# Optimization experiments

Measured on AMD Instinct MI355X. Metric: run time of the kernel, lower is better.

The kernel has to match this reference:

```python
import math
import jax, jax.numpy as jnp
import numpy as np

B, L, H, E = 16, 2048, 8, 64
FACTOR = 1


def setup_inputs() -> dict:
    key = jax.random.key(0)
    kq, kk, kv = jax.random.split(key, 3)
    queries = jax.random.normal(kq, (B, L, H, E), dtype=jnp.float32)
    keys = jax.random.normal(kk, (B, L, H, E), dtype=jnp.float32)
    values = jax.random.normal(kv, (B, L, H, E), dtype=jnp.float32)
    return {"queries": queries, "keys": keys, "values": values, "attn_mask": 0}


def reference(queries, keys, values, attn_mask):
    # queries/keys/values: [B, L, H, E]; attn_mask is unused (as in the original).
    b, l, h, e = queries.shape
    # [B, H, E, L]
    qp = jnp.transpose(queries, (0, 2, 3, 1))
    kp = jnp.transpose(keys, (0, 2, 3, 1))
    vp = jnp.transpose(values, (0, 2, 3, 1))

    # Period-based dependency discovery via FFT cross-correlation.
    qf = jnp.fft.rfft(qp, axis=-1)
    kf = jnp.fft.rfft(kp, axis=-1)
    corr = jnp.fft.irfft(qf * jnp.conj(kf), n=l, axis=-1)  # [B, H, E, L]

    # Inference-style time-delay aggregation (per-batch top-k delays).
    top_k = max(1, int(FACTOR * math.log(l)))
    mean_value = corr.mean(axis=(1, 2))  # [B, L]
    weights, delay = jax.lax.top_k(mean_value, top_k)  # [B, K]
    tmp_corr = jax.nn.softmax(weights, axis=-1)  # [B, K]

    # Gather from doubled tensor == circular roll: index (t + delay) mod L.
    idx = (jnp.arange(l)[None, None, :] + delay[:, :, None]) % l  # [B, K, L]
    # vp[:, None]: [B, 1, H, E, L]; idx broadcast to [B, K, 1, 1, L]
    pattern = jnp.take_along_axis(vp[:, None], idx[:, :, None, None, :], axis=-1)  # [B, K, H, E, L]
    agg = jnp.einsum('bkhel,bk->bhel', pattern, tmp_corr)  # [B, H, E, L]

    return jnp.transpose(agg, (0, 3, 1, 2))  # [B, L, H, E]
```

## Files before the change

kernel.cpp:

```cpp
#include <hip/hip_runtime.h>
#include <hip/hip_fp16.h>
#include <cstdint>
#include <cstddef>

#define BB 16
#define LL 2048
#define CC 512
#define TK 7
#define PDC(a) ((a) + ((a) >> 4))
#define PSTR 1056
#define NG 128

typedef float2 cf;
typedef __attribute__((ext_vector_type(4))) float f32x4v;

__device__ inline cf cadd(cf a, cf b){ return make_float2(a.x + b.x, a.y + b.y); }
__device__ inline cf csub(cf a, cf b){ return make_float2(a.x - b.x, a.y - b.y); }
__device__ inline cf cmul(cf a, cf b){ return make_float2(a.x*b.x - a.y*b.y, a.x*b.y + a.y*b.x); }

template<int S> __device__ inline cf crot(cf z){
  return (S < 0) ? make_float2(z.y, -z.x) : make_float2(-z.y, z.x);
}

template<int S> __device__ inline void dft4(cf* x){
  const cf t0 = cadd(x[0], x[2]), t1 = csub(x[0], x[2]);
  const cf t2 = cadd(x[1], x[3]), t3 = csub(x[1], x[3]);
  const cf r = crot<S>(t3);
  x[0] = cadd(t0, t2); x[2] = csub(t0, t2);
  x[1] = cadd(t1, r);  x[3] = csub(t1, r);
}

template<int S> __device__ inline void dft8(cf* x){
  cf e[4] = { x[0], x[2], x[4], x[6] };
  cf o[4] = { x[1], x[3], x[5], x[7] };
  dft4<S>(e); dft4<S>(o);
  const float H = 0.70710678118654752440f;
  o[1] = cmul(o[1], make_float2(H, (float)S * H));
  o[2] = crot<S>(o[2]);
  o[3] = cmul(o[3], make_float2(-H, (float)S * H));
  x[0] = cadd(e[0], o[0]); x[4] = csub(e[0], o[0]);
  x[1] = cadd(e[1], o[1]); x[5] = csub(e[1], o[1]);
  x[2] = cadd(e[2], o[2]); x[6] = csub(e[2], o[2]);
  x[3] = cadd(e[3], o[3]); x[7] = csub(e[3], o[3]);
}

struct Tw { cf w2[7], w3[7], w4a[3], w4b[3]; };

template<int S>
__device__ inline void make_tw(int tid, Tw& T){
  const float base = (float)S * 6.283185307179586f / 2048.0f;
  const int j7 = tid & 7, j63 = tid & 63;
#pragma unroll
  for (int i = 0; i < 7; ++i){
    float s, c;
    __sincosf(base * (float)(32 * (i + 1) * j7), &s, &c);  T.w2[i] = make_float2(c, s);
    __sincosf(base * (float)( 4 * (i + 1) * j63), &s, &c); T.w3[i] = make_float2(c, s);
  }
#pragma unroll
  for (int i = 0; i < 3; ++i){
    float s, c;
    __sincosf(base * (float)((i + 1) * tid), &s, &c);         T.w4a[i] = make_float2(c, s);
    __sincosf(base * (float)((i + 1) * (tid + 256)), &s, &c); T.w4b[i] = make_float2(c, s);
  }
}

template<int S>
__device__ inline void fft_s123(cf* Bc, cf* Cc, cf* x, const Tw& T, int tid){
  dft8<S>(x);
#pragma unroll
  for (int t = 0; t < 8; ++t) Bc[PDC((tid << 3) + t)] = x[t];
  __syncthreads();
  {
    cf y[8];
#pragma unroll
    for (int t = 0; t < 8; ++t) y[t] = Bc[PDC(tid + (t << 8))];
#pragma unroll
    for (int t = 1; t < 8; ++t) y[t] = cmul(y[t], T.w2[t - 1]);
    dft8<S>(y);
    const int base = ((tid >> 3) << 6) + (tid & 7);
#pragma unroll
    for (int t = 0; t < 8; ++t) Cc[PDC(base + (t << 3))] = y[t];
  }
  __syncthreads();
  {
    cf y[8];
#pragma unroll
    for (int t = 0; t < 8; ++t) y[t] = Cc[PDC(tid + (t << 8))];
#pragma unroll
    for (int t = 1; t < 8; ++t) y[t] = cmul(y[t], T.w3[t - 1]);
    dft8<S>(y);
    const int base = ((tid >> 6) << 9) + (tid & 63);
#pragma unroll
    for (int t = 0; t < 8; ++t) Bc[PDC(base + (t << 6))] = y[t];
  }
  __syncthreads();
}

__global__ __launch_bounds__(256) void transpose_pack(const float* __restrict__ q,
                                                      const float* __restrict__ k,
                                                      __half2* __restrict__ z){
  int bid = blockIdx.x;
  const int tt = bid & 31; bid >>= 5;
  const int ct = bid & 7;  bid >>= 3;
  const int b = bid;
  const int t0 = tt << 6, c0 = ct << 6;
  __shared__ __half2 T[64][69];
  const int tid = threadIdx.x;
  const size_t inbase = ((size_t)b * LL + t0) * CC + c0;
  const int c4 = (tid & 15) << 2;
  f32x4v a[4], e[4];
#pragma unroll
  for (int p2 = 0; p2 < 4; ++p2){
    const int row = (p2 << 4) + (tid >> 4);
    a[p2] = __builtin_nontemporal_load(
        reinterpret_cast<const f32x4v*>(q + inbase + (size_t)row * CC + c4));
    e[p2] = __builtin_nontemporal_load(
        reinterpret_cast<const f32x4v*>(k + inbase + (size_t)row * CC + c4));
  }
#pragma unroll
  for (int p2 = 0; p2 < 4; ++p2){
    const int row = (p2 << 4) + (tid >> 4);
    T[row][c4 + 0] = __floats2half2_rn(a[p2][0], e[p2][0]);
    T[row][c4 + 1] = __floats2half2_rn(a[p2][1], e[p2][1]);
    T[row][c4 + 2] = __floats2half2_rn(a[p2][2], e[p2][2]);
    T[row][c4 + 3] = __floats2half2_rn(a[p2][3], e[p2][3]);
  }
  __syncthreads();
  const size_t outbase = ((size_t)b * CC + c0) * LL + (size_t)t0;
#pragma unroll
  for (int it = 0; it < 4; ++it){
    const int idx = (it << 8) + tid;
    const int c = idx >> 4;
    const int t4 = (idx & 15) << 2;
    const __half2 u0 = T[t4 + 0][c], u1 = T[t4 + 1][c];
    const __half2 u2 = T[t4 + 2][c], u3 = T[t4 + 3][c];
    uint4 w;
    w.x = *reinterpret_cast<const uint*>(&u0);
    w.y = *reinterpret_cast<const uint*>(&u1);
    w.z = *reinterpret_cast<const uint*>(&u2);
    w.w = *reinterpret_cast<const uint*>(&u3);
    *reinterpret_cast<uint4*>(&z[outbase + (size_t)c * LL + t4]) = w;
  }
}

__global__ __launch_bounds__(256) void fft_fwd(const __half2* __restrict__ z,
                                               float2* __restrict__ Ppart){
  int bid = blockIdx.x;
  const int g = bid & (NG - 1); const int b = bid >> 7;
  const int tid = threadIdx.x;
  __shared__ cf B[2176];
  Tw T; make_tw<-1>(tid, T);
  const __half2* zg = z + (((size_t)b * CC + (size_t)g * 4) << 11);
  float accRe[4] = {0,0,0,0};
  float accIm[4] = {0,0,0,0};
  float acc1024 = 0.f;
  __half2 h[8];
#pragma unroll
  for (int t = 0; t < 8; ++t) h[t] = zg[tid + (t << 8)];
  for (int ch = 0; ch < 4; ++ch){
    cf x[8];
#pragma unroll
    for (int t = 0; t < 8; ++t) x[t] = __half22float2(h[t]);
    if (ch < 3){
      const __half2* zn = zg + ((size_t)(ch + 1) << 11);
#pragma unroll
      for (int t = 0; t < 8; ++t) h[t] = zn[tid + (t << 8)];
    }
    dft8<-1>(x);
    __syncthreads();
#pragma unroll
    for (int t = 0; t < 8; ++t) B[PDC((tid << 3) + t)] = x[t];
    __syncthreads();
    cf y[8];
#pragma unroll
    for (int t = 0; t < 8; ++t) y[t] = B[PDC(tid + (t << 8))];
#pragma unroll
    for (int t = 1; t < 8; ++t) y[t] = cmul(y[t], T.w2[t - 1]);
    dft8<-1>(y);
    __syncthreads();
    {
      const int base = ((tid >> 3) << 6) + (tid & 7);
#pragma unroll
      for (int t = 0; t < 8; ++t) B[PDC(base + (t << 3))] = y[t];
    }
    __syncthreads();
#pragma unroll
    for (int t = 0; t < 8; ++t) y[t] = B[PDC(tid + (t << 8))];
#pragma unroll
    for (int t = 1; t < 8; ++t) y[t] = cmul(y[t], T.w3[t - 1]);
    dft8<-1>(y);
    __syncthreads();
    {
      const int base = ((tid >> 6) << 9) + (tid & 63);
#pragma unroll
      for (int t = 0; t < 8; ++t) B[PDC(base + (t << 6))] = y[t];
    }
    __syncthreads();
    cf y0[4], y1[4];
#pragma unroll
    for (int t = 0; t < 4; ++t) y0[t] = B[PDC(tid + (t << 9))];
#pragma unroll
    for (int t = 0; t < 4; ++t) y1[t] = B[PDC(tid + 256 + (t << 9))];
#pragma unroll
    for (int t = 1; t < 4; ++t){
      y0[t] = cmul(y0[t], T.w4a[t - 1]);
      y1[t] = cmul(y1[t], T.w4b[t - 1]);
    }
    dft4<-1>(y0); dft4<-1>(y1);
#pragma unroll
    for (int t = 0; t < 4; ++t) B[PDC(tid + (t << 9))] = y0[t];
#pragma unroll
    for (int t = 0; t < 4; ++t) B[PDC(tid + 256 + (t << 9))] = y1[t];
    __syncthreads();
    const cf Areg[4] = { y0[0], y1[0], y0[1], y1[1] };
#pragma unroll
    for (int r = 0; r < 4; ++r){
      const int f = tid + (r << 8);
      const int p = (2048 - f) & 2047;
      const cf A = Areg[r];
      const cf Bv = B[PDC(p)];
      accRe[r] += 0.5f  * (Bv.y * A.x + Bv.x * A.y);
      accIm[r] += 0.25f * (A.x * A.x + A.y * A.y - Bv.x * Bv.x - Bv.y * Bv.y);
    }
    if (tid == 0){
      const cf A = y0[2];
      acc1024 += A.x * A.y;
    }
  }
  float2* pp = Ppart + ((size_t)b * NG + g) * PSTR;
#pragma unroll
  for (int r = 0; r < 4; ++r)
    pp[tid + (r << 8)] = make_float2(accRe[r], accIm[r]);
  if (tid == 0) pp[1024] = make_float2(acc1024, 0.f);
}

__global__ __launch_bounds__(256) void reduce_P(const float2* __restrict__ Ppart,
                                                float2* __restrict__ P){
  const int gid = blockIdx.x * 256 + threadIdx.x;
  const int b = gid >> 11, f = gid & 2047;
  const int src = (f <= 1024) ? f : 2048 - f;
  const float sgn = (f <= 1024) ? 1.f : -1.f;
  float sr = 0.f, si = 0.f;
#pragma unroll 8
  for (int g = 0; g < NG; ++g){
    const float2 v = Ppart[((size_t)b * NG + g) * PSTR + src];
    sr += v.x; si += v.y;
  }
  P[((size_t)b << 11) + f] = make_float2(sr, sgn * si);
}

__global__ __launch_bounds__(256) void fft_inv_topk(const float2* __restrict__ P,
                                                    int* __restrict__ delays,
                                                    float* __restrict__ probs){
  const int b = blockIdx.x;
  const int tid = threadIdx.x;
  __shared__ cf Bc[2176];
  __shared__ cf Cc[2176];
  __shared__ float vals[2048];
  __shared__ float rv[256]; __shared__ int ri[256];
  __shared__ float wsel[TK]; __shared__ int dsel[TK];
  Tw T; make_tw<1>(tid, T);
  cf x[8];
#pragma unroll
  for (int t = 0; t < 8; ++t) x[t] = P[((size_t)b << 11) + tid + (t << 8)];
  fft_s123<1>(Bc, Cc, x, T, tid);
  const float scale = 1.0f / (2048.0f * 512.0f);
  {
#pragma unroll
    for (int hh = 0; hh < 2; ++hh){
      const int j = tid + (hh << 8);
      cf y[4];
#pragma unroll
      for (int t = 0; t < 4; ++t) y[t] = Bc[PDC(j + (t << 9))];
      const cf* w = hh ? T.w4b : T.w4a;
#pragma unroll
      for (int t = 1; t < 4; ++t) y[t] = cmul(y[t], w[t - 1]);
      dft4<1>(y);
#pragma unroll
      for (int t = 0; t < 4; ++t) vals[j + (t << 9)] = y[t].x * scale;
    }
  }
  __syncthreads();
  for (int kk = 0; kk < TK; ++kk){
    float best = -1e30f; int bi = LL;
    for (int i = tid; i < LL; i += 256){
      const float xv = vals[i];
      if (xv > best){ best = xv; bi = i; }
    }
    rv[tid] = best; ri[tid] = bi;
    __syncthreads();
    for (int s = 128; s > 0; s >>= 1){
      if (tid < s){
        const float ov = rv[tid + s]; const int oi = ri[tid + s];
        if (ov > rv[tid] || (ov == rv[tid] && oi < ri[tid])){ rv[tid] = ov; ri[tid] = oi; }
      }
      __syncthreads();
    }
    if (tid == 0){ wsel[kk] = rv[0]; dsel[kk] = ri[0]; vals[ri[0]] = -1e30f; }
    __syncthreads();
  }
  if (tid == 0){
    const float m = wsel[0];
    float e[TK], ssum = 0.f;
#pragma unroll
    for (int i = 0; i < TK; ++i){ e[i] = expf(wsel[i] - m); ssum += e[i]; }
    const float inv = 1.0f / ssum;
#pragma unroll
    for (int i = 0; i < TK; ++i){
      probs[b * TK + i] = e[i] * inv;
      delays[b * TK + i] = dsel[i];
    }
  }
}

__global__ __launch_bounds__(256) void agg_out(const float* __restrict__ v,
                                               const int* __restrict__ delays,
                                               const float* __restrict__ probs,
                                               float* __restrict__ out){
  const int bid = blockIdx.x;
  const int xcd = bid & 7;
  const int j0  = bid >> 3;
  const int tid = threadIdx.x;
  const int row_off = tid >> 7;
  const int slot = tid & 127;
  const int b0 = xcd << 1;
  float p0[TK], p1[TK]; int d0[TK], d1[TK];
#pragma unroll
  for (int k = 0; k < TK; ++k){
    p0[k] = probs[b0 * TK + k];        d0[k] = delays[b0 * TK + k];
    p1[k] = probs[(b0 + 1) * TK + k];  d1[k] = delays[(b0 + 1) * TK + k];
  }
  const f32x4v* v4 = reinterpret_cast<const f32x4v*>(v);
  f32x4v A[TK], Bv[TK];

#define AGG_ISSUE(s, X)                                                       \
  {                                                                           \
    const int it_ = j0 + ((s) << 8);                                          \
    const int seg_ = it_ >> 10;                                               \
    const int b_ = b0 + seg_;                                                 \
    const int t_ = ((it_ << 1) + row_off) & (LL - 1);                         \
    _Pragma("unroll")                                                         \
    for (int k = 0; k < TK; ++k){                                             \
      const int dk_ = seg_ ? d1[k] : d0[k];                                   \
      const int src_ = (t_ + dk_) & (LL - 1);                                 \
      X[k] = v4[(((size_t)((b_ << 11) + src_)) << 7) + slot];                 \
    }                                                                         \
  }

  AGG_ISSUE(0, A);
#pragma unroll
  for (int s = 0; s < 8; ++s){
    if (s & 1){ if (s < 7) AGG_ISSUE(s + 1, A); }
    else      { if (s < 7) AGG_ISSUE(s + 1, Bv); }
    const int it = j0 + (s << 8);
    const int seg = it >> 10;
    const int b = b0 + seg;
    const int t = ((it << 1) + row_off) & (LL - 1);
    f32x4v acc = {0.f, 0.f, 0.f, 0.f};
    if (s & 1){
#pragma unroll
      for (int k = 0; k < TK; ++k) acc += Bv[k] * (seg ? p1[k] : p0[k]);
    } else {
#pragma unroll
      for (int k = 0; k < TK; ++k) acc += A[k] * (seg ? p1[k] : p0[k]);
    }
    f32x4v* o = reinterpret_cast<f32x4v*>(out) + (((size_t)((b << 11) + t)) << 7) + slot;
    __builtin_nontemporal_store(acc, o);
  }
#undef AGG_ISSUE
}

extern "C" void kernel_launch(void* const* d_in, const int* in_sizes, int n_in,
                              void* d_out, int out_size, void* d_ws, size_t ws_size,
                              hipStream_t stream){
  const float* q = (const float*)d_in[0];
  const float* k = (const float*)d_in[1];
  const float* v = (const float*)d_in[2];
  float* out = (float*)d_out;

  char* ws = (char*)d_ws;
  const size_t Z_BYTES  = (size_t)BB * CC * LL * sizeof(__half2);
  const size_t PP_BYTES = (size_t)BB * NG * PSTR * sizeof(float2);
  const size_t P_BYTES  = (size_t)BB * LL * sizeof(float2);
  __half2* zbuf = (__half2*)ws;
  float2* Ppart = (float2*)(ws + Z_BYTES);
  float2* Pbuf  = (float2*)(ws + Z_BYTES + PP_BYTES);
  int* delays = (int*)(ws + Z_BYTES + PP_BYTES + P_BYTES);
  float* probs = (float*)(ws + Z_BYTES + PP_BYTES + P_BYTES + 1024);

  hipLaunchKernelGGL(transpose_pack, dim3(BB * 32 * 8), dim3(256), 0, stream, q, k, zbuf);
  hipLaunchKernelGGL(fft_fwd, dim3(BB * NG), dim3(256), 0, stream, zbuf, Ppart);
  hipLaunchKernelGGL(reduce_P, dim3((BB * LL) / 256), dim3(256), 0, stream, Ppart, Pbuf);
  hipLaunchKernelGGL(fft_inv_topk, dim3(BB), dim3(256), 0, stream, Pbuf, delays, probs);
  hipLaunchKernelGGL(agg_out, dim3(2048), dim3(256), 0, stream,
                     v, delays, probs, out);
}
```

Before: 133.4 us.

## Stage shifted value rows through LDS with async global_load_lds double buffering

The aggregation kernel now loads the seven delayed value rows into LDS with global_load_lds, double-buffered with explicit vmcnt waits and barriers, in place of register-resident prefetch. Each block now handles one batch over a contiguous block of 16 time steps, so probs and delays are read once into shared memory. The aim is to cut register pressure and let more loads stay in flight. The cost is two barriers per stage, LDS traffic, and a large shared buffer that may lower occupancy.

```diff
diff --git a/kernel.cpp b/kernel.cpp
--- a/kernel.cpp
+++ b/kernel.cpp
@@ -320,54 +320,70 @@
   const int bid = blockIdx.x;
   const int xcd = bid & 7;
   const int j0  = bid >> 3;
+  const int b   = (xcd << 1) + (j0 >> 7);
+  const int tbase = (j0 & 127) << 4;
   const int tid = threadIdx.x;
+  const int wid = tid >> 6;
+  const int lane = tid & 63;
+  __shared__ float buf[2][28 * 256];
+  __shared__ float psh[TK];
+  __shared__ int dsh[TK];
+  if (tid < TK){
+    psh[tid] = probs[b * TK + tid];
+    dsh[tid] = delays[b * TK + tid];
+  }
+  __syncthreads();
+
+  const char* vbytes = (const char*)v;
+  const size_t brow = ((size_t)b) << 11;
+
+#define AGG_STAGE(s, cur)                                                     \
+  {                                                                           \
+    const int t0_ = tbase + ((s) << 1);                                       \
+    _Pragma("unroll")                                                         \
+    for (int i_ = 0; i_ < 7; ++i_){                                           \
+      const int c_ = wid * 7 + i_;                                            \
+      const int row2_ = (c_ >= 14) ? 1 : 0;                                   \
+      const int rem_ = c_ - row2_ * 14;                                       \
+      const int k_ = rem_ >> 1, h_ = rem_ & 1;                                \
+      const int ts_ = (t0_ + row2_ + dsh[k_]) & (LL - 1);                     \
+      const char* g_ = vbytes + (((size_t)(brow + ts_)) << 11) +              \
+                       (h_ << 10) + (lane << 4);                              \
+      char* lp_ = (char*)&buf[cur][0] + c_ * 1024;                            \
+      __builtin_amdgcn_global_load_lds(                                       \
+          (const __attribute__((address_space(1))) void*)g_,                  \
+          (__attribute__((address_space(3))) void*)lp_, 16, 0, 0);            \
+    }                                                                         \
+  }
+
+  AGG_STAGE(0, 0);
   const int row_off = tid >> 7;
   const int slot = tid & 127;
-  const int b0 = xcd << 1;
-  float p0[TK], p1[TK]; int d0[TK], d1[TK];
-#pragma unroll
-  for (int k = 0; k < TK; ++k){
-    p0[k] = probs[b0 * TK + k];        d0[k] = delays[b0 * TK + k];
-    p1[k] = probs[(b0 + 1) * TK + k];  d1[k] = delays[(b0 + 1) * TK + k];
-  }
-  const f32x4v* v4 = reinterpret_cast<const f32x4v*>(v);
-  f32x4v A[TK], Bv[TK];
-
-#define AGG_ISSUE(s, X)                                                       \
-  {                                                                           \
-    const int it_ = j0 + ((s) << 8);                                          \
-    const int seg_ = it_ >> 10;                                               \
-    const int b_ = b0 + seg_;                                                 \
-    const int t_ = ((it_ << 1) + row_off) & (LL - 1);                         \
-    _Pragma("unroll")                                                         \
-    for (int k = 0; k < TK; ++k){                                             \
-      const int dk_ = seg_ ? d1[k] : d0[k];                                   \
-      const int src_ = (t_ + dk_) & (LL - 1);                                 \
-      X[k] = v4[(((size_t)((b_ << 11) + src_)) << 7) + slot];                 \
-    }                                                                         \
-  }
-
-  AGG_ISSUE(0, A);
+  const int lbase_off = row_off * 14 + (slot >> 6);
+  const int lbyte = (slot & 63) << 4;
 #pragma unroll
   for (int s = 0; s < 8; ++s){
-    if (s & 1){ if (s < 7) AGG_ISSUE(s + 1, A); }
-    else      { if (s < 7) AGG_ISSUE(s + 1, Bv); }
-    const int it = j0 + (s << 8);
-    const int seg = it >> 10;
-    const int b = b0 + seg;
-    const int t = ((it << 1) + row_off) & (LL - 1);
+    const int cur = s & 1;
+    if (s < 7){
+      AGG_STAGE(s + 1, cur ^ 1);
+      asm volatile("s_waitcnt vmcnt(7)" ::: "memory");
+    } else {
+      asm volatile("s_waitcnt vmcnt(0)" ::: "memory");
+    }
+    __syncthreads();
     f32x4v acc = {0.f, 0.f, 0.f, 0.f};
-    if (s & 1){
-#pragma unroll
-      for (int k = 0; k < TK; ++k) acc += Bv[k] * (seg ? p1[k] : p0[k]);
-    } else {
-#pragma unroll
-      for (int k = 0; k < TK; ++k) acc += A[k] * (seg ? p1[k] : p0[k]);
-    }
-    f32x4v* o = reinterpret_cast<f32x4v*>(out) + (((size_t)((b << 11) + t)) << 7) + slot;
+#pragma unroll
+    for (int k = 0; k < TK; ++k){
+      const f32x4v xv = *reinterpret_cast<const f32x4v*>(
+          (const char*)&buf[cur][0] + (lbase_off + (k << 1)) * 1024 + lbyte);
+      acc += xv * psh[k];
+    }
+    const int t = tbase + (s << 1) + row_off;
+    f32x4v* o = reinterpret_cast<f32x4v*>(out + ((brow + t) << 9)) + slot;
     __builtin_nontemporal_store(acc, o);
-  }
-#undef AGG_ISSUE
+    __syncthreads();
+  }
+#undef AGG_STAGE
 }
 
 extern "C" void kernel_launch(void* const* d_in, const int* in_sizes, int n_in,
```

Result: faster. 123.2 us (-7.7%).
